# Kernel optimization log

Measured on AMD Instinct MI355X. Metric: run time of the kernel, lower is better.

Reference implementation:

```python
import jax, jax.numpy as jnp
import numpy as np

NH = 16  # num_attention_heads
DH = 64  # attention_head_size
HID = NH * DH
TYPE_VOCAB = 2


def setup_inputs() -> dict:
    key = jax.random.key(0)
    ks = jax.random.split(key, 10)
    B, S = 4, 2048
    s = 0.02
    return {
        "hidden_states": jax.random.normal(ks[0], (B, S, HID), jnp.float32),
        "attention_mask": jnp.zeros((B, 1, 1, S), jnp.float32),
        "seg_ids": jax.random.randint(ks[1], (B, S), 0, TYPE_VOCAB),
        "Wq": jax.random.normal(ks[2], (HID, HID), jnp.float32) * s,
        "bq": jnp.zeros((HID,), jnp.float32),
        "Wk": jax.random.normal(ks[3], (HID, HID), jnp.float32) * s,  # key has NO bias (F.linear with weight only)
        "Wv": jax.random.normal(ks[4], (HID, HID), jnp.float32) * s,
        "bv": jnp.zeros((HID,), jnp.float32),
        "seg_table": jax.random.normal(ks[5], (TYPE_VOCAB, HID), jnp.float32) * s,
        "b_q_s": jnp.zeros((1, NH, 1, DH), jnp.float32),
    }


def reference(hidden_states, attention_mask, seg_ids, Wq, bq, Wk, Wv, bv, seg_table, b_q_s):
    B, S, H = hidden_states.shape
    # QKV projections (key projection has no bias, matching F.linear(x, key.weight))
    q = hidden_states @ Wq.T + bq
    k = hidden_states @ Wk.T
    v = hidden_states @ Wv.T + bv
    # [B, NH, S, DH]
    q = q.reshape(B, S, NH, DH).transpose(0, 2, 1, 3)
    k = k.reshape(B, S, NH, DH).transpose(0, 2, 1, 3)
    v = v.reshape(B, S, NH, DH).transpose(0, 2, 1, 3)
    scale = 1.0 / np.sqrt(DH).astype(np.float32)
    scores = jnp.einsum('bhid,bhjd->bhij', q * scale, k)
    # segment-embedding bias: seg_rep [B, S, NH, DH]
    seg_rep = seg_table[seg_ids].reshape(B, S, NH, DH)
    qs = jnp.einsum('bhid,bjhd->bhij', q + b_q_s, seg_rep)
    scores = scores + qs + attention_mask
    probs = jax.nn.softmax(scores, axis=-1)  # dropout: eval mode (identity)
    ctx = jnp.einsum('bhij,bhjd->bihd', probs, v).reshape(B, S, H)
    return ctx
```

## Files before the change

### kernel.cpp

```cpp
#include <hip/hip_runtime.h>
#include <cstdint>
#include <cmath>

#define RLN2 1.44269504088896340736f

typedef __attribute__((ext_vector_type(8))) short short8;
typedef __attribute__((ext_vector_type(4))) float f32x4;
typedef __attribute__((ext_vector_type(16))) float f32x16;
typedef __attribute__((ext_vector_type(4))) unsigned int uint4v;

__device__ __forceinline__ unsigned short f2bf(float f) {
  unsigned int u = __float_as_uint(f);
  u += 0x7fffu + ((u >> 16) & 1u);
  return (unsigned short)(u >> 16);
}

__device__ __forceinline__ unsigned int cvt_pk_bf16(float lo, float hi) {
  unsigned int r;
  asm("v_cvt_pk_bf16_f32 %0, %1, %2" : "=v"(r) : "v"(lo), "v"(hi));
  return r;
}

__device__ __forceinline__ float fast_exp2(float x) {
#if __has_builtin(__builtin_amdgcn_exp2f)
  return __builtin_amdgcn_exp2f(x);
#else
  return exp2f(x);
#endif
}

__device__ __forceinline__ void gload16(const void* g, void* l) {
  __builtin_amdgcn_global_load_lds(
      (const __attribute__((address_space(1))) unsigned int*)g,
      (__attribute__((address_space(3))) unsigned int*)l,
      16, 0, 0);
}


__global__ void __launch_bounds__(256) k_cvt_hs(const float* __restrict__ src,
                                                unsigned short* __restrict__ dst) {
  size_t i = (size_t)blockIdx.x * 256 + threadIdx.x;
  const float4* s = (const float4*)src + i * 2;
  float4 a = s[0], b = s[1];
  short8 o;
  o[0] = (short)f2bf(a.x); o[1] = (short)f2bf(a.y); o[2] = (short)f2bf(a.z); o[3] = (short)f2bf(a.w);
  o[4] = (short)f2bf(b.x); o[5] = (short)f2bf(b.y); o[6] = (short)f2bf(b.z); o[7] = (short)f2bf(b.w);
  ((short8*)dst)[i] = o;
}

__global__ void __launch_bounds__(256) k_cvt_w(const float* __restrict__ Wq,
                                               const float* __restrict__ Wk,
                                               const float* __restrict__ Wv,
                                               unsigned short* __restrict__ dst) {
  size_t i = (size_t)blockIdx.x * 256 + threadIdx.x;
  int e = (int)(i * 8);
  int n = e >> 10, c = e & 1023;
  const float* row = (n < 1024) ? (Wq + (size_t)n * 1024)
                   : (n < 2048) ? (Wk + (size_t)(n - 1024) * 1024)
                                : (Wv + (size_t)(n - 2048) * 1024);
  const float4* s = (const float4*)(row + c);
  float4 a = s[0], b = s[1];
  short8 o;
  o[0] = (short)f2bf(a.x); o[1] = (short)f2bf(a.y); o[2] = (short)f2bf(a.z); o[3] = (short)f2bf(a.w);
  o[4] = (short)f2bf(b.x); o[5] = (short)f2bf(b.y); o[6] = (short)f2bf(b.z); o[7] = (short)f2bf(b.w);
  ((short8*)dst)[i] = o;
}

__global__ void __launch_bounds__(256) k_seg(const int* __restrict__ seg_ids,
                                             const float* __restrict__ seg_table,
                                             unsigned short* __restrict__ Kaug) {
  size_t i = (size_t)blockIdx.x * 256 + threadIdx.x;
  int e = (int)(i * 8);
  int jl = e >> 10;
  int r  = e & 1023;
  int sid = seg_ids[jl];
  const float4* s = (const float4*)(seg_table + (size_t)sid * 1024 + r);
  float4 a = s[0], b = s[1];
  short8 o;
  o[0] = (short)f2bf(a.x); o[1] = (short)f2bf(a.y); o[2] = (short)f2bf(a.z); o[3] = (short)f2bf(a.w);
  o[4] = (short)f2bf(b.x); o[5] = (short)f2bf(b.y); o[6] = (short)f2bf(b.z); o[7] = (short)f2bf(b.w);
  int b_ = jl >> 11, j = jl & 2047;
  int h = r >> 6, d = r & 63;
  size_t off = ((size_t)(b_ * 16 + h) * 2048 + j) * 128 + 64 + d;
  *(short8*)(Kaug + off) = o;
}

__global__ void __launch_bounds__(256) k_vt(const unsigned short* __restrict__ V,
                                            unsigned short* __restrict__ Vt) {
  __shared__ unsigned short lt[64 * 72];
  int blk = blockIdx.x;
  int bh = blk >> 5, jt = blk & 31;
  int j0 = jt * 64;
  int tid = threadIdx.x;
  const char* src = (const char*)(V + ((size_t)bh * 2048 + j0) * 64);
#pragma unroll
  for (int it = 0; it < 2; ++it) {
    int c = tid + it * 256;
    int j = c >> 3, colb = (c & 7) * 16;
    int kh2 = (j >> 5) & 1, c2 = (j >> 3) & 3, hi2 = (j >> 2) & 1, r2 = j & 3;
    int jpos = (2 * kh2 + (c2 >> 1)) * 16 + 8 * hi2 + 4 * (c2 & 1) + r2;
    short8 v = *(const short8*)(src + (size_t)j * 128 + colb);
    int d0 = colb >> 1;
#pragma unroll
    for (int e = 0; e < 8; ++e)
      lt[(d0 + e) * 72 + jpos] = (unsigned short)v[e];
  }
  __syncthreads();
  char* dst = (char*)(Vt + (size_t)bh * 131072 + j0);
#pragma unroll
  for (int it = 0; it < 2; ++it) {
    int c = tid + it * 256;
    int d = c >> 3, jc = (c & 7) * 8;
    short8 o = *(const short8*)&lt[d * 72 + jc];
    *(short8*)(dst + (size_t)d * 4096 + jc * 2) = o;
  }
}

__global__ void __launch_bounds__(256) k_gemm(const unsigned short* __restrict__ A,
                                              const unsigned short* __restrict__ Bw,
                                              const float* __restrict__ bq,
                                              const float* __restrict__ bv,
                                              const float* __restrict__ bqs,
                                              unsigned short* __restrict__ Qaug,
                                              unsigned short* __restrict__ Kaug,
                                              unsigned short* __restrict__ Vo) {
  __shared__ unsigned short As[128 * 32];
  __shared__ unsigned short Bs[128 * 32];
  int n0 = blockIdx.x * 128;
  int m0 = blockIdx.y * 128;
  int tid = threadIdx.x;
  int w = tid >> 6, lane = tid & 63;
  int wr = (w >> 1) * 64, wc = (w & 1) * 64;
  int rA = lane & 15;
  int kg = (lane >> 4) * 16;
  f32x4 acc[4][4] = {};
  const char* Ab = (const char*)A;
  const char* Bb = (const char*)Bw;

  for (int kt = 0; kt < 32; ++kt) {
    int kb0 = kt * 64;
#pragma unroll
    for (int c = 0; c < 2; ++c) {
      int chunk = w * 2 + c;
      int y = chunk * 1024 + lane * 16;
      int row = y >> 6, colb = y & 63;
      gload16(Ab + (size_t)(m0 + row) * 2048 + kb0 + colb, (char*)As + chunk * 1024);
      gload16(Bb + (size_t)(n0 + row) * 2048 + kb0 + colb, (char*)Bs + chunk * 1024);
    }
    __syncthreads();
    short8 af[4], bfr[4];
#pragma unroll
    for (int m = 0; m < 4; ++m)
      af[m] = *(const short8*)((const char*)As + (wr + m * 16 + rA) * 64 + kg);
#pragma unroll
    for (int n = 0; n < 4; ++n)
      bfr[n] = *(const short8*)((const char*)Bs + (wc + n * 16 + rA) * 64 + kg);
#pragma unroll
    for (int m = 0; m < 4; ++m)
#pragma unroll
      for (int n = 0; n < 4; ++n)
        acc[m][n] = __builtin_amdgcn_mfma_f32_16x16x32_bf16(af[m], bfr[n], acc[m][n], 0, 0, 0);
    __syncthreads();
  }

  int seg = n0 >> 10;
  int colbase = n0 & 1023;
#pragma unroll
  for (int n = 0; n < 4; ++n) {
    int o = colbase + wc + n * 16 + (lane & 15);
    int h = o >> 6, d = o & 63;
    float bias = 0.f, bqsv = 0.f;
    if (seg == 0) { bias = bq[o]; bqsv = bqs[o]; }
    else if (seg == 2) { bias = bv[o]; }
#pragma unroll
    for (int m = 0; m < 4; ++m) {
#pragma unroll
      for (int r = 0; r < 4; ++r) {
        int i = m0 + wr + m * 16 + (lane >> 4) * 4 + r;
        int b_ = i >> 11, sdx = i & 2047;
        float val = acc[m][n][r];
        size_t tok = (size_t)(b_ * 16 + h) * 2048 + sdx;
        if (seg == 0) {
          float qv = val + bias;
          Qaug[tok * 128 + d]      = f2bf(qv * (0.125f * RLN2));
          Qaug[tok * 128 + 64 + d] = f2bf((qv + bqsv) * RLN2);
        } else if (seg == 1) {
          Kaug[tok * 128 + d] = f2bf(val);
        } else {
          Vo[tok * 64 + d] = f2bf(val + bias);
        }
      }
    }
  }
}

__global__ void __launch_bounds__(256, 3) k_attn(const unsigned short* __restrict__ Qaug,
                                                 const unsigned short* __restrict__ Kaug,
                                                 const unsigned short* __restrict__ Vt,
                                                 const float* __restrict__ mask,
                                                 float* __restrict__ out) {
  __shared__ char smem[49152];
  char* Ksb = smem;
  char* Vsb = smem + 32768;

  int qt = blockIdx.x, h = blockIdx.y, b_ = blockIdx.z;
  int bh = b_ * 16 + h;
  int i0 = qt * 128;
  int tid = threadIdx.x, w = tid >> 6, lane = tid & 63;
  int q = lane & 31, hi = lane >> 5;
  int swzq = (q & 7) << 4;
  const char* Qg = (const char*)Qaug + (size_t)bh * 2048 * 256;
  const char* Kg = (const char*)Kaug + (size_t)bh * 2048 * 256;
  const char* Vg = (const char*)Vt + (size_t)bh * 64 * 4096;
  const float* maskb = mask + (size_t)b_ * 2048;

  int foff[8];
#pragma unroll
  for (int ds = 0; ds < 8; ++ds)
    foff[ds] = (ds * 32 + hi * 16) ^ swzq;

  int kst_row = lane >> 4, kst_x = (lane & 15) * 16;
  int vst_dv = lane >> 3;
  int vst_x = ((lane & 7) * 16) ^ ((vst_dv & 7) << 4);

#pragma unroll
  for (int c = 0; c < 4; ++c) {
    int ck = w * 4 + c;
    int krow = ck * 4 + kst_row;
    gload16(Kg + (size_t)krow * 256 + (kst_x ^ ((krow & 7) << 4)), Ksb + ck * 1024);
  }
#pragma unroll
  for (int c = 0; c < 2; ++c) {
    int ck = w * 2 + c;
    int dv = ck * 8 + vst_dv;
    gload16(Vg + (size_t)dv * 4096 + vst_x, Vsb + ck * 1024);
  }

  short8 qf[8];
  {
    const char* qrow = Qg + (size_t)(i0 + w * 32 + q) * 256 + hi * 16;
#pragma unroll
    for (int ds = 0; ds < 8; ++ds)
      qf[ds] = *(const short8*)(qrow + ds * 32);
  }
  __syncthreads();

  float m_run = -1e30f, l_run = 0.f;
  f32x16 accO[2] = {};

  for (int t = 0; t < 32; ++t) {
    int cur = t & 1, nxt = cur ^ 1;
    int j0 = t * 64;
    if (t < 31) {
      int jn = j0 + 64;
      char* kd = Ksb + nxt * 16384;
      char* vd = Vsb + nxt * 8192;
#pragma unroll
      for (int c = 0; c < 4; ++c) {
        int ck = w * 4 + c;
        int krow = ck * 4 + kst_row;
        gload16(Kg + (size_t)(jn + krow) * 256 + (kst_x ^ ((krow & 7) << 4)), kd + ck * 1024);
      }
#pragma unroll
      for (int c = 0; c < 2; ++c) {
        int ck = w * 2 + c;
        int dv = ck * 8 + vst_dv;
        gload16(Vg + (size_t)dv * 4096 + jn * 2 + vst_x, vd + ck * 1024);
      }
    }
    const char* kq = Ksb + cur * 16384 + q * 256;
    const char* vq = Vsb + cur * 8192 + q * 128;

    f32x16 s0 = {}, s1 = {};
    __builtin_amdgcn_s_setprio(1);
#pragma unroll
    for (int ds = 0; ds < 8; ++ds) {
      short8 kf0 = *(const short8*)(kq + foff[ds]);
      short8 kf1 = *(const short8*)(kq + foff[ds] + 8192);
      s0 = __builtin_amdgcn_mfma_f32_32x32x16_bf16(kf0, qf[ds], s0, 0, 0, 0);
      s1 = __builtin_amdgcn_mfma_f32_32x32x16_bf16(kf1, qf[ds], s1, 0, 0, 0);
    }
    __builtin_amdgcn_s_setprio(0);

#pragma unroll
    for (int c = 0; c < 4; ++c) {
      f32x4 mv0 = *(const f32x4*)(maskb + j0 + 8 * c + 4 * hi);
      f32x4 mv1 = *(const f32x4*)(maskb + j0 + 32 + 8 * c + 4 * hi);
#pragma unroll
      for (int r = 0; r < 4; ++r) {
        s0[4 * c + r] += mv0[r] * RLN2;
        s1[4 * c + r] += mv1[r] * RLN2;
      }
    }

    float tm = -1e30f;
#pragma unroll
    for (int i = 0; i < 16; ++i) tm = fmaxf(tm, fmaxf(s0[i], s1[i]));
    tm = fmaxf(tm, __shfl_xor(tm, 32));

    if (__any(tm > m_run + 8.0f)) {
      float mn = fmaxf(m_run, tm);
      float alpha = fast_exp2(m_run - mn);
      m_run = mn;
      l_run *= alpha;
#pragma unroll
      for (int i = 0; i < 16; ++i) { accO[0][i] *= alpha; accO[1][i] *= alpha; }
    }

    float ps = 0.f;
#pragma unroll
    for (int i = 0; i < 16; ++i) {
      float e0 = fast_exp2(s0[i] - m_run);
      float e1 = fast_exp2(s1[i] - m_run);
      s0[i] = e0; s1[i] = e1;
      ps += e0 + e1;
    }
    ps += __shfl_xor(ps, 32);
    l_run += ps;

    uint4v pk[4];
#pragma unroll
    for (int ks = 0; ks < 4; ++ks) {
      int o = 8 * (ks & 1);
      const f32x16& sv = (ks < 2) ? s0 : s1;
      pk[ks][0] = cvt_pk_bf16(sv[o + 0], sv[o + 1]);
      pk[ks][1] = cvt_pk_bf16(sv[o + 2], sv[o + 3]);
      pk[ks][2] = cvt_pk_bf16(sv[o + 4], sv[o + 5]);
      pk[ks][3] = cvt_pk_bf16(sv[o + 6], sv[o + 7]);
    }

    __builtin_amdgcn_s_setprio(1);
#pragma unroll
    for (int ks = 0; ks < 4; ++ks) {
      short8 pf = __builtin_bit_cast(short8, pk[ks]);
      short8 vf0 = *(const short8*)(vq + foff[ks]);
      short8 vf1 = *(const short8*)(vq + foff[ks] + 4096);
      accO[0] = __builtin_amdgcn_mfma_f32_32x32x16_bf16(vf0, pf, accO[0], 0, 0, 0);
      accO[1] = __builtin_amdgcn_mfma_f32_32x32x16_bf16(vf1, pf, accO[1], 0, 0, 0);
    }
    __builtin_amdgcn_s_setprio(0);
    __syncthreads();
  }

  float inv = 1.0f / l_run;
  float* orow = out + ((size_t)b_ * 2048 + i0 + w * 32 + q) * 1024 + h * 64;
#pragma unroll
  for (int vh = 0; vh < 2; ++vh) {
#pragma unroll
    for (int c = 0; c < 4; ++c) {
      f32x4 o;
      o[0] = accO[vh][4 * c + 0] * inv;
      o[1] = accO[vh][4 * c + 1] * inv;
      o[2] = accO[vh][4 * c + 2] * inv;
      o[3] = accO[vh][4 * c + 3] * inv;
      *(f32x4*)(orow + vh * 32 + 8 * c + 4 * hi) = o;
    }
  }
}

extern "C" void kernel_launch(void* const* d_in, const int* in_sizes, int n_in,
                              void* d_out, int out_size, void* d_ws, size_t ws_size,
                              hipStream_t stream) {
  (void)in_sizes; (void)n_in; (void)out_size; (void)ws_size;
  const float* hs        = (const float*)d_in[0];
  const float* mask      = (const float*)d_in[1];
  const int*   seg_ids   = (const int*)d_in[2];
  const float* Wq        = (const float*)d_in[3];
  const float* bq        = (const float*)d_in[4];
  const float* Wk        = (const float*)d_in[5];
  const float* Wv        = (const float*)d_in[6];
  const float* bv        = (const float*)d_in[7];
  const float* seg_table = (const float*)d_in[8];
  const float* bqs       = (const float*)d_in[9];
  float* out = (float*)d_out;
  char* ws = (char*)d_ws;

  unsigned short* hsb  = (unsigned short*)(ws + 0);
  unsigned short* Wcat = (unsigned short*)(ws + 16777216);
  unsigned short* Qaug = (unsigned short*)(ws + 23068672);
  unsigned short* Kaug = (unsigned short*)(ws + 56623104);
  unsigned short* V    = (unsigned short*)(ws + 90177536);
  unsigned short* Vt   = (unsigned short*)(ws + 0);

  k_cvt_hs<<<dim3(4096), dim3(256), 0, stream>>>(hs, hsb);
  k_cvt_w<<<dim3(1536), dim3(256), 0, stream>>>(Wq, Wk, Wv, Wcat);
  k_gemm<<<dim3(24, 64), dim3(256), 0, stream>>>(hsb, Wcat, bq, bv, bqs, Qaug, Kaug, V);
  k_seg<<<dim3(4096), dim3(256), 0, stream>>>(seg_ids, seg_table, Kaug);
  k_vt<<<dim3(2048), dim3(256), 0, stream>>>(V, Vt);
  k_attn<<<dim3(16, 16, 4), dim3(256), 0, stream>>>(Qaug, Kaug, Vt, mask, out);
}
```

Measured before the change: 280.4 us.

## Fuse V transpose into GEMM epilogue, single-buffer V, prescale mask, tree reductions

The QKV GEMM epilogue now writes V directly in the transposed, permuted layout the attention kernel expects, which removes the separate transpose kernel and its extra pass over memory. The mask is premultiplied by log2(e) once inside the segment kernel, so the attention loop skips that multiply. In attention, V uses a single shared-memory buffer loaded after the PV MFMAs with an extra barrier, cutting LDS to 40KB so launch bounds can target 4 blocks per CU. Row max and sum use tree reductions. The cost is less overlap of V loads with compute and an added synchronisation per tile.

```diff
diff --git a/kernel.cpp b/kernel.cpp
--- a/kernel.cpp
+++ b/kernel.cpp
@@ -5,6 +5,7 @@
 #define RLN2 1.44269504088896340736f
 
 typedef __attribute__((ext_vector_type(8))) short short8;
+typedef __attribute__((ext_vector_type(4))) short short4v;
 typedef __attribute__((ext_vector_type(4))) float f32x4;
 typedef __attribute__((ext_vector_type(16))) float f32x16;
 typedef __attribute__((ext_vector_type(4))) unsigned int uint4v;
@@ -68,11 +69,14 @@
 
 __global__ void __launch_bounds__(256) k_seg(const int* __restrict__ seg_ids,
                                              const float* __restrict__ seg_table,
-                                             unsigned short* __restrict__ Kaug) {
+                                             const float* __restrict__ mask,
+                                             unsigned short* __restrict__ Kaug,
+                                             float* __restrict__ mask2) {
   size_t i = (size_t)blockIdx.x * 256 + threadIdx.x;
   int e = (int)(i * 8);
   int jl = e >> 10;
   int r  = e & 1023;
+  if (r == 0) mask2[jl] = mask[jl] * RLN2;
   int sid = seg_ids[jl];
   const float4* s = (const float4*)(seg_table + (size_t)sid * 1024 + r);
   float4 a = s[0], b = s[1];
@@ -85,37 +89,6 @@
   *(short8*)(Kaug + off) = o;
 }
 
-__global__ void __launch_bounds__(256) k_vt(const unsigned short* __restrict__ V,
-                                            unsigned short* __restrict__ Vt) {
-  __shared__ unsigned short lt[64 * 72];
-  int blk = blockIdx.x;
-  int bh = blk >> 5, jt = blk & 31;
-  int j0 = jt * 64;
-  int tid = threadIdx.x;
-  const char* src = (const char*)(V + ((size_t)bh * 2048 + j0) * 64);
-#pragma unroll
-  for (int it = 0; it < 2; ++it) {
-    int c = tid + it * 256;
-    int j = c >> 3, colb = (c & 7) * 16;
-    int kh2 = (j >> 5) & 1, c2 = (j >> 3) & 3, hi2 = (j >> 2) & 1, r2 = j & 3;
-    int jpos = (2 * kh2 + (c2 >> 1)) * 16 + 8 * hi2 + 4 * (c2 & 1) + r2;
-    short8 v = *(const short8*)(src + (size_t)j * 128 + colb);
-    int d0 = colb >> 1;
-#pragma unroll
-    for (int e = 0; e < 8; ++e)
-      lt[(d0 + e) * 72 + jpos] = (unsigned short)v[e];
-  }
-  __syncthreads();
-  char* dst = (char*)(Vt + (size_t)bh * 131072 + j0);
-#pragma unroll
-  for (int it = 0; it < 2; ++it) {
-    int c = tid + it * 256;
-    int d = c >> 3, jc = (c & 7) * 8;
-    short8 o = *(const short8*)&lt[d * 72 + jc];
-    *(short8*)(dst + (size_t)d * 4096 + jc * 2) = o;
-  }
-}
-
 __global__ void __launch_bounds__(256) k_gemm(const unsigned short* __restrict__ A,
                                               const unsigned short* __restrict__ Bw,
                                               const float* __restrict__ bq,
@@ -123,7 +96,7 @@
                                               const float* __restrict__ bqs,
                                               unsigned short* __restrict__ Qaug,
                                               unsigned short* __restrict__ Kaug,
-                                              unsigned short* __restrict__ Vo) {
+                                              unsigned short* __restrict__ Vt) {
   __shared__ unsigned short As[128 * 32];
   __shared__ unsigned short Bs[128 * 32];
   int n0 = blockIdx.x * 128;
@@ -165,6 +138,7 @@
 
   int seg = n0 >> 10;
   int colbase = n0 & 1023;
+  int g = lane >> 4;
 #pragma unroll
   for (int n = 0; n < 4; ++n) {
     int o = colbase + wc + n * 16 + (lane & 15);
@@ -174,32 +148,42 @@
     else if (seg == 2) { bias = bv[o]; }
 #pragma unroll
     for (int m = 0; m < 4; ++m) {
-#pragma unroll
-      for (int r = 0; r < 4; ++r) {
-        int i = m0 + wr + m * 16 + (lane >> 4) * 4 + r;
+      if (seg == 2) {
+        int i = m0 + wr + m * 16 + g * 4;
         int b_ = i >> 11, sdx = i & 2047;
-        float val = acc[m][n][r];
-        size_t tok = (size_t)(b_ * 16 + h) * 2048 + sdx;
-        if (seg == 0) {
-          float qv = val + bias;
-          Qaug[tok * 128 + d]      = f2bf(qv * (0.125f * RLN2));
-          Qaug[tok * 128 + 64 + d] = f2bf((qv + bqsv) * RLN2);
-        } else if (seg == 1) {
-          Kaug[tok * 128 + d] = f2bf(val);
-        } else {
-          Vo[tok * 64 + d] = f2bf(val + bias);
+        int bh = b_ * 16 + h;
+        int pos = (sdx & ~63) + 32 * ((m >> 1) & 1) + 16 * (m & 1) + 8 * (g & 1) + 4 * ((g >> 1) & 1);
+        short4v pv;
+#pragma unroll
+        for (int r = 0; r < 4; ++r)
+          pv[r] = (short)f2bf(acc[m][n][r] + bias);
+        *(short4v*)(Vt + (size_t)bh * 131072 + (size_t)d * 2048 + pos) = pv;
+      } else {
+#pragma unroll
+        for (int r = 0; r < 4; ++r) {
+          int i = m0 + wr + m * 16 + g * 4 + r;
+          int b_ = i >> 11, sdx = i & 2047;
+          float val = acc[m][n][r];
+          size_t tok = (size_t)(b_ * 16 + h) * 2048 + sdx;
+          if (seg == 0) {
+            float qv = val + bias;
+            Qaug[tok * 128 + d]      = f2bf(qv * (0.125f * RLN2));
+            Qaug[tok * 128 + 64 + d] = f2bf((qv + bqsv) * RLN2);
+          } else {
+            Kaug[tok * 128 + d] = f2bf(val);
+          }
         }
       }
     }
   }
 }
 
-__global__ void __launch_bounds__(256, 3) k_attn(const unsigned short* __restrict__ Qaug,
+__global__ void __launch_bounds__(256, 4) k_attn(const unsigned short* __restrict__ Qaug,
                                                  const unsigned short* __restrict__ Kaug,
                                                  const unsigned short* __restrict__ Vt,
-                                                 const float* __restrict__ mask,
+                                                 const float* __restrict__ mask2,
                                                  float* __restrict__ out) {
-  __shared__ char smem[49152];
+  __shared__ char smem[40960];
   char* Ksb = smem;
   char* Vsb = smem + 32768;
 
@@ -212,7 +196,7 @@
   const char* Qg = (const char*)Qaug + (size_t)bh * 2048 * 256;
   const char* Kg = (const char*)Kaug + (size_t)bh * 2048 * 256;
   const char* Vg = (const char*)Vt + (size_t)bh * 64 * 4096;
-  const float* maskb = mask + (size_t)b_ * 2048;
+  const float* maskb = mask2 + (size_t)b_ * 2048;
 
   int foff[8];
 #pragma unroll
@@ -251,25 +235,18 @@
   for (int t = 0; t < 32; ++t) {
     int cur = t & 1, nxt = cur ^ 1;
     int j0 = t * 64;
+
     if (t < 31) {
       int jn = j0 + 64;
       char* kd = Ksb + nxt * 16384;
-      char* vd = Vsb + nxt * 8192;
 #pragma unroll
       for (int c = 0; c < 4; ++c) {
         int ck = w * 4 + c;
         int krow = ck * 4 + kst_row;
         gload16(Kg + (size_t)(jn + krow) * 256 + (kst_x ^ ((krow & 7) << 4)), kd + ck * 1024);
       }
-#pragma unroll
-      for (int c = 0; c < 2; ++c) {
-        int ck = w * 2 + c;
-        int dv = ck * 8 + vst_dv;
-        gload16(Vg + (size_t)dv * 4096 + jn * 2 + vst_x, vd + ck * 1024);
-      }
     }
     const char* kq = Ksb + cur * 16384 + q * 256;
-    const char* vq = Vsb + cur * 8192 + q * 128;
 
     f32x16 s0 = {}, s1 = {};
     __builtin_amdgcn_s_setprio(1);
@@ -288,35 +265,48 @@
       f32x4 mv1 = *(const f32x4*)(maskb + j0 + 32 + 8 * c + 4 * hi);
 #pragma unroll
       for (int r = 0; r < 4; ++r) {
-        s0[4 * c + r] += mv0[r] * RLN2;
-        s1[4 * c + r] += mv1[r] * RLN2;
-      }
-    }
-
-    float tm = -1e30f;
-#pragma unroll
-    for (int i = 0; i < 16; ++i) tm = fmaxf(tm, fmaxf(s0[i], s1[i]));
-    tm = fmaxf(tm, __shfl_xor(tm, 32));
-
-    if (__any(tm > m_run + 8.0f)) {
-      float mn = fmaxf(m_run, tm);
-      float alpha = fast_exp2(m_run - mn);
-      m_run = mn;
-      l_run *= alpha;
-#pragma unroll
-      for (int i = 0; i < 16; ++i) { accO[0][i] *= alpha; accO[1][i] *= alpha; }
-    }
-
-    float ps = 0.f;
-#pragma unroll
-    for (int i = 0; i < 16; ++i) {
-      float e0 = fast_exp2(s0[i] - m_run);
-      float e1 = fast_exp2(s1[i] - m_run);
-      s0[i] = e0; s1[i] = e1;
-      ps += e0 + e1;
-    }
-    ps += __shfl_xor(ps, 32);
-    l_run += ps;
+        s0[4 * c + r] += mv0[r];
+        s1[4 * c + r] += mv1[r];
+      }
+    }
+
+    {
+      f32x16 mx;
+#pragma unroll
+      for (int i = 0; i < 16; ++i) mx[i] = fmaxf(s0[i], s1[i]);
+#pragma unroll
+      for (int i = 0; i < 8; ++i) mx[i] = fmaxf(mx[i], mx[i + 8]);
+#pragma unroll
+      for (int i = 0; i < 4; ++i) mx[i] = fmaxf(mx[i], mx[i + 4]);
+      float tm = fmaxf(fmaxf(mx[0], mx[1]), fmaxf(mx[2], mx[3]));
+      tm = fmaxf(tm, __shfl_xor(tm, 32));
+
+      if (__any(tm > m_run + 8.0f)) {
+        float mn = fmaxf(m_run, tm);
+        float alpha = fast_exp2(m_run - mn);
+        m_run = mn;
+        l_run *= alpha;
+#pragma unroll
+        for (int i = 0; i < 16; ++i) { accO[0][i] *= alpha; accO[1][i] *= alpha; }
+      }
+    }
+    {
+      f32x16 es;
+#pragma unroll
+      for (int i = 0; i < 16; ++i) {
+        float e0 = fast_exp2(s0[i] - m_run);
+        float e1 = fast_exp2(s1[i] - m_run);
+        s0[i] = e0; s1[i] = e1;
+        es[i] = e0 + e1;
+      }
+#pragma unroll
+      for (int i = 0; i < 8; ++i) es[i] += es[i + 8];
+#pragma unroll
+      for (int i = 0; i < 4; ++i) es[i] += es[i + 4];
+      float ps = (es[0] + es[1]) + (es[2] + es[3]);
+      ps += __shfl_xor(ps, 32);
+      l_run += ps;
+    }
 
     uint4v pk[4];
 #pragma unroll
@@ -329,6 +319,9 @@
       pk[ks][3] = cvt_pk_bf16(sv[o + 6], sv[o + 7]);
     }
 
+    __syncthreads();
+
+    const char* vq = Vsb + q * 128;
     __builtin_amdgcn_s_setprio(1);
 #pragma unroll
     for (int ks = 0; ks < 4; ++ks) {
@@ -339,7 +332,18 @@
       accO[1] = __builtin_amdgcn_mfma_f32_32x32x16_bf16(vf1, pf, accO[1], 0, 0, 0);
     }
     __builtin_amdgcn_s_setprio(0);
+
     __syncthreads();
+
+    if (t < 31) {
+      int jn = j0 + 64;
+#pragma unroll
+      for (int c = 0; c < 2; ++c) {
+        int ck = w * 2 + c;
+        int dv = ck * 8 + vst_dv;
+        gload16(Vg + (size_t)dv * 4096 + jn * 2 + vst_x, Vsb + ck * 1024);
+      }
+    }
   }
 
   float inv = 1.0f / l_run;
@@ -379,13 +383,12 @@
   unsigned short* Wcat = (unsigned short*)(ws + 16777216);
   unsigned short* Qaug = (unsigned short*)(ws + 23068672);
   unsigned short* Kaug = (unsigned short*)(ws + 56623104);
-  unsigned short* V    = (unsigned short*)(ws + 90177536);
-  unsigned short* Vt   = (unsigned short*)(ws + 0);
+  unsigned short* Vt   = (unsigned short*)(ws + 90177536);
+  float*          mask2 = (float*)(ws + 0);
 
   k_cvt_hs<<<dim3(4096), dim3(256), 0, stream>>>(hs, hsb);
   k_cvt_w<<<dim3(1536), dim3(256), 0, stream>>>(Wq, Wk, Wv, Wcat);
-  k_gemm<<<dim3(24, 64), dim3(256), 0, stream>>>(hsb, Wcat, bq, bv, bqs, Qaug, Kaug, V);
-  k_seg<<<dim3(4096), dim3(256), 0, stream>>>(seg_ids, seg_table, Kaug);
-  k_vt<<<dim3(2048), dim3(256), 0, stream>>>(V, Vt);
-  k_attn<<<dim3(16, 16, 4), dim3(256), 0, stream>>>(Qaug, Kaug, Vt, mask, out);
-}
+  k_gemm<<<dim3(24, 64), dim3(256), 0, stream>>>(hsb, Wcat, bq, bv, bqs, Qaug, Kaug, Vt);
+  k_seg<<<dim3(4096), dim3(256), 0, stream>>>(seg_ids, seg_table, mask, Kaug, mask2);
+  k_attn<<<dim3(16, 16, 4), dim3(256), 0, stream>>>(Qaug, Kaug, Vt, mask2, out);
+}
```

New measurement: 333.4 us. 1.19x slower.
